# Performance work log

Measured on AMD Instinct MI355X. Metric: run time of the kernel, lower is better.

Reference implementation:

```python
import jax, jax.numpy as jnp
import numpy as np

B, L, D = 4, 2048, 64
N_HEAD = 4
LOCALITY = 0.2
PI = 3.141592653589793


def setup_inputs() -> dict:
    key = jax.random.key(0)
    k1, k2, k3 = jax.random.split(key, 3)
    mesh = jax.random.uniform(k1, (B, L, 2), dtype=jnp.float32)
    inputs = jax.random.normal(k2, (B, L, D), dtype=jnp.float32)
    lmda = jax.random.uniform(k3, (N_HEAD, 1, 1), dtype=jnp.float32)
    return {"mesh": mesh, "inputs": inputs, "lmda": lmda}


def reference(mesh, inputs, lmda):
    FMAX = jnp.finfo(jnp.float32).max
    # pairwise squared distances: (B, L, L)
    diff = mesh[:, :, None, :] - mesh[:, None, :, :]
    m_dist = jnp.sum(diff * diff, axis=-1)
    # per-head scale in (0, inf): tan(pi/4 * (1-eps) * (1 + sin(lmda)))
    scale = jnp.tan(0.25 * PI * (1.0 - 1e-07) * (1.0 + jnp.sin(lmda)))  # (H,1,1)
    scaled = m_dist[:, None, :, :] * scale  # (B, H, L, L)
    # row-wise quantile threshold (linear interpolation, matching torch.quantile)
    thresh = jnp.quantile(scaled, LOCALITY, axis=-1, keepdims=True)  # (B,H,L,1)
    masked = jnp.where(scaled <= thresh, scaled, FMAX)
    att = jax.nn.softmax(-masked, axis=-1)  # (B, H, L, L)
    # aggregate: (B,H,L,L) x (B,L,D) -> (B,L,H,D) -> (B,L,H*D)
    conv = jnp.einsum('bhnj,bjd->bnhd', att, inputs)
    conv = conv.reshape(inputs.shape[0], -1, N_HEAD * inputs.shape[-1])
    return jnp.concatenate([inputs, conv], axis=-1)
```

## Files before the change

### kernel.cpp

```cpp
#include <hip/hip_runtime.h>
#include <math.h>

#ifndef M_PI
#define M_PI 3.14159265358979323846
#endif

namespace {
constexpr int B_ = 4;
constexpr int L_ = 2048;
constexpr int D_ = 64;
constexpr int H_ = 4;
constexpr int RB = 8;
constexpr int KT = 64;
constexpr int NTILE = L_ / KT;
constexpr int CAPC = 256;
constexpr int OUTW = D_ + H_ * D_;
constexpr int APS = 2064;
}

typedef __attribute__((ext_vector_type(8))) short bf16x8;
typedef __attribute__((ext_vector_type(4))) float f32x4;

__device__ __forceinline__ unsigned bf16_rne(float x) {
    unsigned u = __float_as_uint(x);
    return (u + 0x7fffu + ((u >> 16) & 1u)) >> 16;
}

#define LDS_FENCE() __builtin_amdgcn_s_waitcnt(0xC07F)

__global__ __launch_bounds__(256) void prep_kernel(const float* __restrict__ inputs,
                                                   char* __restrict__ ws) {
    const int blk = blockIdx.x;
    const int b = blk >> 6;
    const int r6 = blk & 63;
    const int tile = r6 >> 2;
    const int qr = r6 & 3;
    const int t = threadIdx.x;
    const float* inb = inputs + ((size_t)b * L_ + tile * 128) * D_;
    char* wsb = ws + (size_t)b * (L_ * D_ * 2) + tile * (128 * D_ * 2);
    #pragma unroll
    for (int i = 0; i < 4; ++i) {
        const int idx = qr * 1024 + i * 256 + t;
        const int n  = idx & 63;
        const int kp = idx >> 6;
        const int kl = kp << 1;
        const float x0 = inb[kl * D_ + n];
        const float x1 = inb[(kl + 1) * D_ + n];
        const unsigned a = bf16_rne(x0);
        const unsigned c = bf16_rne(x1);
        const int chunk = (kl >> 3) * 64 + n;
        const int e = kl & 7;
        *reinterpret_cast<unsigned*>(wsb + chunk * 16 + e * 2) = a | (c << 16);
    }
}

__global__ __launch_bounds__(512, 8) void posatt_kernel(
    const float* __restrict__ mesh,
    const float* __restrict__ inputs,
    const float* __restrict__ lmda,
    const char* __restrict__ ws,
    float* __restrict__ out)
{
    __shared__ __align__(16) float2 s_mesh[L_];
    __shared__ __align__(16) char s_u1[16448];
    __shared__ float s_scale[H_];
    __shared__ float s_th[RB][H_];
    __shared__ float s_d409[RB], s_d410[RB];
    __shared__ float s_wsum[RB][H_];
    __shared__ unsigned s_ccw[8];

    const int t = threadIdx.x;
    const int l = t & 63;
    const int w = t >> 6;
    const int blk = blockIdx.x;
    const int b = blk >> 8;
    const int n0 = (blk & 255) * RB;

    const float2* meshg = reinterpret_cast<const float2*>(mesh) + (size_t)b * L_;

    if (t < H_) {
        const double lam = (double)lmda[t];
        const float C = (float)(0.25 * M_PI * (1.0 - 1e-07));
        const float s1 = (float)sin(lam);
        const float arg = __fmul_rn(C, __fadd_rn(1.0f, s1));
        s_scale[t] = (float)tan((double)arg);
    }
    if (t < RB) { s_d409[t] = 0.0f; s_d410[t] = 0.0f; }
    {
        const float4* mg = reinterpret_cast<const float4*>(mesh + (size_t)b * L_ * 2);
        float4* msd = reinterpret_cast<float4*>(s_mesh);
        msd[t] = mg[t];
        msd[t + 512] = mg[t + 512];
    }
    __syncthreads();

    {
        unsigned* hw = reinterpret_cast<unsigned*>(s_u1) + w * 256;
        float* cw = reinterpret_cast<float*>(s_u1 + 8192) + w * CAPC;
        const int rl = w;
        const float2 me = meshg[n0 + rl];
        *reinterpret_cast<uint4*>(&hw[l * 4]) = make_uint4(0u, 0u, 0u, 0u);
        if (l == 0) s_ccw[w] = 0u;
        LDS_FENCE();
        #pragma unroll 4
        for (int it = 0; it < 32; ++it) {
            const int j = (it << 6) + l;
            const float2 mj = meshg[j];
            const float dx = __fsub_rn(me.x, mj.x);
            const float dy = __fsub_rn(me.y, mj.y);
            const float d = __fadd_rn(__fmul_rn(dx, dx), __fmul_rn(dy, dy));
            int bin = (int)(d * 128.0f); bin = bin < 255 ? bin : 255;
            atomicAdd(&hw[bin], 1u);
        }
        LDS_FENCE();
        int lo, hi; unsigned base;
        {
            const uint4 hv = *reinterpret_cast<const uint4*>(&hw[l * 4]);
            const unsigned p0 = hv.x, p1 = p0 + hv.y, p2 = p1 + hv.z, p3 = p2 + hv.w;
            unsigned sc = p3;
            #pragma unroll
            for (int off = 1; off < 64; off <<= 1) {
                const unsigned uu = __shfl_up(sc, off);
                if (l >= off) sc += uu;
            }
            const unsigned eb = sc - p3;
            const unsigned cum[4] = {eb + p0, eb + p1, eb + p2, eb + p3};
            int flo = -1, fhi = -1; unsigned fbase = 0u;
            #pragma unroll
            for (int e = 0; e < 4; ++e) {
                const unsigned prev = e ? cum[e - 1] : eb;
                if (cum[e] > 409u && prev <= 409u) { flo = l * 4 + e; fbase = prev; }
                if (cum[e] > 410u && prev <= 410u) { fhi = l * 4 + e; }
            }
            const unsigned long long bmlo = __ballot(flo >= 0);
            const int srclo = (int)__builtin_ctzll(bmlo);
            lo = __shfl(flo, srclo);
            base = __shfl(fbase, srclo);
            const unsigned long long bmhi = __ballot(fhi >= 0);
            hi = __shfl(fhi, (int)__builtin_ctzll(bmhi));
        }
        #pragma unroll 4
        for (int it = 0; it < 32; ++it) {
            const int j = (it << 6) + l;
            const float2 mj = meshg[j];
            const float dx = __fsub_rn(me.x, mj.x);
            const float dy = __fsub_rn(me.y, mj.y);
            const float d = __fadd_rn(__fmul_rn(dx, dx), __fmul_rn(dy, dy));
            int bin = (int)(d * 128.0f); bin = bin < 255 ? bin : 255;
            if (bin >= lo && bin <= hi) {
                const unsigned p = atomicAdd(&s_ccw[w], 1u);
                if (p < (unsigned)CAPC) cw[p] = d;
            }
        }
        LDS_FENCE();
        const int m = (int)min(s_ccw[w], (unsigned)CAPC);
        const unsigned k409 = 409u - base;
        const unsigned k410 = 410u - base;
        const float lo_edge = (float)lo * 0.0078125f;
        const float sc2 = 32768.0f / (float)(hi - lo + 1);
        *reinterpret_cast<uint4*>(&hw[l * 4]) = make_uint4(0u, 0u, 0u, 0u);
        LDS_FENCE();
        #pragma unroll 2
        for (int ci = l; ci < m; ci += 64) {
            const float v = cw[ci];
            int b2 = (int)(__fmul_rn(__fsub_rn(v, lo_edge), sc2));
            b2 = b2 < 255 ? b2 : 255; b2 = b2 > 0 ? b2 : 0;
            atomicAdd(&hw[b2], 1u);
        }
        LDS_FENCE();
        int lo2, hi2; unsigned base2;
        {
            const uint4 hv = *reinterpret_cast<const uint4*>(&hw[l * 4]);
            const unsigned p0 = hv.x, p1 = p0 + hv.y, p2 = p1 + hv.z, p3 = p2 + hv.w;
            unsigned sc = p3;
            #pragma unroll
            for (int off = 1; off < 64; off <<= 1) {
                const unsigned uu = __shfl_up(sc, off);
                if (l >= off) sc += uu;
            }
            const unsigned eb = sc - p3;
            const unsigned cum[4] = {eb + p0, eb + p1, eb + p2, eb + p3};
            int flo = -1, fhi = -1; unsigned fbase = 0u;
            #pragma unroll
            for (int e = 0; e < 4; ++e) {
                const unsigned prev = e ? cum[e - 1] : eb;
                if (cum[e] > k409 && prev <= k409) { flo = l * 4 + e; fbase = prev; }
                if (cum[e] > k410 && prev <= k410) { fhi = l * 4 + e; }
            }
            const unsigned long long bmlo = __ballot(flo >= 0);
            const int srclo = (int)__builtin_ctzll(bmlo);
            lo2 = __shfl(flo, srclo);
            base2 = __shfl(fbase, srclo);
            const unsigned long long bmhi = __ballot(fhi >= 0);
            hi2 = __shfl(fhi, (int)__builtin_ctzll(bmhi));
        }
        if (l == 0) s_ccw[w] = 0u;
        LDS_FENCE();
        float* c2 = reinterpret_cast<float*>(hw);
        #pragma unroll 2
        for (int ci = l; ci < m; ci += 64) {
            const float v = cw[ci];
            int b2 = (int)(__fmul_rn(__fsub_rn(v, lo_edge), sc2));
            b2 = b2 < 255 ? b2 : 255; b2 = b2 > 0 ? b2 : 0;
            if (b2 >= lo2 && b2 <= hi2) {
                const unsigned p = atomicAdd(&s_ccw[w], 1u);
                if (p < 256u) c2[p] = v;
            }
        }
        LDS_FENCE();
        const int c = (int)min(s_ccw[w], 256u);
        const int q409 = (int)(k409 - base2);
        const int q410 = (int)(k410 - base2);
        #pragma unroll 1
        for (int cc0 = 0; cc0 < c; cc0 += 64) {
            const int ci = cc0 + l;
            const float v = (ci < c) ? c2[ci] : 0.0f;
            int lt = 0, le = 0;
            #pragma unroll 4
            for (int i = 0; i < c; ++i) {
                const float u = c2[i];
                lt += (u < v) ? 1 : 0;
                le += (u <= v) ? 1 : 0;
            }
            if (ci < c) {
                if (lt <= q409 && q409 < le) s_d409[rl] = v;
                if (lt <= q410 && q410 < le) s_d410[rl] = v;
            }
        }
    }
    __syncthreads();

    if (t < RB * H_) {
        const int r = t >> 2, h = t & 3;
        const float scl = s_scale[h];
        const float s409 = __fmul_rn(s_d409[r], scl);
        const float s410 = __fmul_rn(s_d410[r], scl);
        const float pos = 0.2f * 2047.0f;
        const float g = pos - 409.0f;
        const float lw = 1.0f - g;
        s_th[r][h] = __fadd_rn(__fmul_rn(s409, lw), __fmul_rn(s410, g));
    }
    __syncthreads();

    const int mr   = t >> 4;
    const int h_b  = mr >> 3;
    const int r_b  = mr & 7;
    const int jg   = t & 15;
    const int row16 = ((h_b & 1) << 3) + r_b;
    const int pln   = h_b >> 1;
    const float2 me_b = s_mesh[n0 + r_b];
    const float sc_b = s_scale[h_b];
    const float th_b = s_th[r_b][h_b];
    const int ks4q_w = jg >> 1;
    const int chunk_w = ks4q_w * 16 + row16;
    const int chunkSw_w = chunk_w ^ (ks4q_w & 7);
    const int aoff = pln * APS + (chunkSw_w << 4) + ((jg & 1) << 3);
    float wacc = 0.0f;

    const int p_w  = w >> 2;
    const int ks_w = (w >> 1) & 1;
    const int nqh  = w & 1;
    const int ks4q_r = ks_w * 4 + (l >> 4);
    const int chunk_r = ks4q_r * 16 + (l & 15);
    const int aroff = p_w * APS + ((chunk_r ^ (ks4q_r & 7)) << 4);
    f32x4 acc[2];
    acc[0] = (f32x4)0.0f; acc[1] = (f32x4)0.0f;

    const float* inpb = inputs + (size_t)b * L_ * D_;
    const char* wsb = ws + (size_t)b * (L_ * D_ * 2);
    char* Abase = s_u1;
    char* Bbase = s_u1 + 2 * APS;

    #pragma unroll 1
    for (int tile = 0; tile < NTILE; ++tile) {
        __syncthreads();
        const uint4 bg = *reinterpret_cast<const uint4*>(wsb + ((size_t)(tile * 512 + t) << 4));
        const int k0 = tile * KT;
        {
            const float4 mq0 = *reinterpret_cast<const float4*>(&s_mesh[k0 + jg * 4]);
            const float4 mq1 = *reinterpret_cast<const float4*>(&s_mesh[k0 + jg * 4 + 2]);
            const float dx0 = __fsub_rn(me_b.x, mq0.x);
            const float dy0 = __fsub_rn(me_b.y, mq0.y);
            const float d0 = __fadd_rn(__fmul_rn(dx0, dx0), __fmul_rn(dy0, dy0));
            const float dx1 = __fsub_rn(me_b.x, mq0.z);
            const float dy1 = __fsub_rn(me_b.y, mq0.w);
            const float d1 = __fadd_rn(__fmul_rn(dx1, dx1), __fmul_rn(dy1, dy1));
            const float dx2 = __fsub_rn(me_b.x, mq1.x);
            const float dy2 = __fsub_rn(me_b.y, mq1.y);
            const float d2 = __fadd_rn(__fmul_rn(dx2, dx2), __fmul_rn(dy2, dy2));
            const float dx3 = __fsub_rn(me_b.x, mq1.z);
            const float dy3 = __fsub_rn(me_b.y, mq1.w);
            const float d3 = __fadd_rn(__fmul_rn(dx3, dx3), __fmul_rn(dy3, dy3));
            const float x0 = __fmul_rn(d0, sc_b);
            const float x1 = __fmul_rn(d1, sc_b);
            const float x2 = __fmul_rn(d2, sc_b);
            const float x3 = __fmul_rn(d3, sc_b);
            const float w0 = (x0 <= th_b) ? __expf(-x0) : 0.0f;
            const float w1 = (x1 <= th_b) ? __expf(-x1) : 0.0f;
            const float w2 = (x2 <= th_b) ? __expf(-x2) : 0.0f;
            const float w3 = (x3 <= th_b) ? __expf(-x3) : 0.0f;
            wacc += (w0 + w1) + (w2 + w3);
            const unsigned u01 = bf16_rne(w0) | (bf16_rne(w1) << 16);
            const unsigned u23 = bf16_rne(w2) | (bf16_rne(w3) << 16);
            *reinterpret_cast<uint2*>(Abase + aoff) = make_uint2(u01, u23);
        }
        *reinterpret_cast<uint4*>(Bbase + t * 16) = bg;
        __syncthreads();
        const bf16x8 afr = *reinterpret_cast<const bf16x8*>(Abase + aroff);
        #pragma unroll
        for (int i = 0; i < 2; ++i) {
            const int nq = nqh * 2 + i;
            const bf16x8 bfr = *reinterpret_cast<const bf16x8*>(
                Bbase + (((ks_w * 4 + (l >> 4)) * 64 + nq * 16 + (l & 15)) << 4));
            acc[i] = __builtin_amdgcn_mfma_f32_16x16x32_bf16(afr, bfr, acc[i], 0, 0, 0);
        }
    }
    __syncthreads();

    wacc += __shfl_xor(wacc, 1);
    wacc += __shfl_xor(wacc, 2);
    wacc += __shfl_xor(wacc, 4);
    wacc += __shfl_xor(wacc, 8);
    if ((l & 15) == 0) s_wsum[r_b][h_b] = wacc;
    {
        float4* Cz = reinterpret_cast<float4*>(s_u1);
        Cz[t] = make_float4(0.f, 0.f, 0.f, 0.f);
    }
    __syncthreads();
    {
        float* Cf = reinterpret_cast<float*>(s_u1);
        #pragma unroll
        for (int i = 0; i < 2; ++i) {
            const int nq = nqh * 2 + i;
            #pragma unroll
            for (int reg = 0; reg < 4; ++reg) {
                const int row = (l >> 4) * 4 + reg;
                const int col = nq * 16 + (l & 15);
                atomicAdd(&Cf[(p_w * 16 + row) * 64 + col], acc[i][reg]);
            }
        }
    }
    __syncthreads();
    {
        const float* Cf = reinterpret_cast<const float*>(s_u1);
        const int pr = t >> 4;
        const int p = pr >> 4;
        const int row16o = pr & 15;
        const int h = p * 2 + (row16o >> 3);
        const int r = row16o & 7;
        const int col = (t & 15) << 2;
        const float wsv = s_wsum[r][h];
        const float inv = (wsv != 0.0f) ? 1.0f / wsv : 0.0f;
        float4 r0 = *reinterpret_cast<const float4*>(&Cf[pr * 64 + col]);
        r0.x *= inv; r0.y *= inv; r0.z *= inv; r0.w *= inv;
        float* op = out + (size_t)(b * L_ + n0 + r) * OUTW + D_ + h * 64 + col;
        *reinterpret_cast<float4*>(op) = r0;
    }
    {
        const int r = t >> 6;
        const int c = t & 63;
        out[(size_t)(b * L_ + n0 + r) * OUTW + c] = inpb[(size_t)(n0 + r) * D_ + c];
    }
}

extern "C" void kernel_launch(void* const* d_in, const int* in_sizes, int n_in,
                              void* d_out, int out_size, void* d_ws, size_t ws_size,
                              hipStream_t stream) {
    const float* mesh   = (const float*)d_in[0];
    const float* inputs = (const float*)d_in[1];
    const float* lmda   = (const float*)d_in[2];
    float* out = (float*)d_out;
    char* ws = (char*)d_ws;
    (void)in_sizes; (void)n_in; (void)out_size; (void)ws_size;
    hipLaunchKernelGGL(prep_kernel, dim3(256), dim3(256), 0, stream, inputs, ws);
    hipLaunchKernelGGL(posatt_kernel, dim3(B_ * (L_ / RB)), dim3(512), 0, stream,
                       mesh, inputs, lmda, ws, out);
}
```

Before: 132.0 us.

## Double-buffer LDS tiles and share distance math across head pairs

Uses two LDS buffers so the MFMA on one tile overlaps with building the weight tile and staging B for the next, cutting the per-tile barriers from two to one. The thread mapping is reworked so each thread computes a distance once and reuses it for two heads. The threshold is compared in unscaled distance space, and exp is replaced by exp2 with a folded log2e scale. Packed bf16 conversion uses v_cvt_pk_bf16_f32. The cost is doubled LDS use and a lower occupancy hint (6 instead of 8), and skipping the per-head scale before the threshold compare may change rounding at the boundary.

```diff
diff --git a/kernel.cpp b/kernel.cpp
--- a/kernel.cpp
+++ b/kernel.cpp
@@ -16,6 +16,9 @@
 constexpr int CAPC = 256;
 constexpr int OUTW = D_ + H_ * D_;
 constexpr int APS = 2064;
+constexpr int ABYTES = 2 * APS;
+constexpr int BBYTES = KT * D_ * 2;
+constexpr int BUFB = ABYTES + BBYTES;
 }
 
 typedef __attribute__((ext_vector_type(8))) short bf16x8;
@@ -25,6 +28,21 @@
     unsigned u = __float_as_uint(x);
     return (u + 0x7fffu + ((u >> 16) & 1u)) >> 16;
 }
+
+__device__ __forceinline__ unsigned cvt_pk_bf16(float lo, float hi) {
+    unsigned r;
+    asm("v_cvt_pk_bf16_f32 %0, %1, %2" : "=v"(r) : "v"(lo), "v"(hi));
+    return r;
+}
+
+#if defined(__has_builtin)
+#if __has_builtin(__builtin_amdgcn_exp2f)
+#define EXP2F(x) __builtin_amdgcn_exp2f(x)
+#endif
+#endif
+#ifndef EXP2F
+#define EXP2F(x) __expf((x) * 0.69314718055994531f)
+#endif
 
 #define LDS_FENCE() __builtin_amdgcn_s_waitcnt(0xC07F)
 
@@ -54,7 +72,7 @@
     }
 }
 
-__global__ __launch_bounds__(512, 8) void posatt_kernel(
+__global__ __launch_bounds__(512, 6) void posatt_kernel(
     const float* __restrict__ mesh,
     const float* __restrict__ inputs,
     const float* __restrict__ lmda,
@@ -62,9 +80,9 @@
     float* __restrict__ out)
 {
     __shared__ __align__(16) float2 s_mesh[L_];
-    __shared__ __align__(16) char s_u1[16448];
+    __shared__ __align__(16) char s_u1[2 * BUFB];
     __shared__ float s_scale[H_];
-    __shared__ float s_th[RB][H_];
+    __shared__ float s_thD[RB];
     __shared__ float s_d409[RB], s_d410[RB];
     __shared__ float s_wsum[RB][H_];
     __shared__ unsigned s_ccw[8];
@@ -230,32 +248,28 @@
     }
     __syncthreads();
 
-    if (t < RB * H_) {
-        const int r = t >> 2, h = t & 3;
-        const float scl = s_scale[h];
-        const float s409 = __fmul_rn(s_d409[r], scl);
-        const float s410 = __fmul_rn(s_d410[r], scl);
+    if (t < RB) {
         const float pos = 0.2f * 2047.0f;
         const float g = pos - 409.0f;
         const float lw = 1.0f - g;
-        s_th[r][h] = __fadd_rn(__fmul_rn(s409, lw), __fmul_rn(s410, g));
-    }
-    __syncthreads();
-
-    const int mr   = t >> 4;
-    const int h_b  = mr >> 3;
-    const int r_b  = mr & 7;
-    const int jg   = t & 15;
-    const int row16 = ((h_b & 1) << 3) + r_b;
-    const int pln   = h_b >> 1;
-    const float2 me_b = s_mesh[n0 + r_b];
-    const float sc_b = s_scale[h_b];
-    const float th_b = s_th[r_b][h_b];
-    const int ks4q_w = jg >> 1;
+        s_thD[t] = __fadd_rn(__fmul_rn(s_d409[t], lw), __fmul_rn(s_d410[t], g));
+    }
+    __syncthreads();
+
+    const int jp = t & 31;
+    const int rr = (t >> 5) & 7;
+    const int h2 = t >> 8;
+    const float2 me_b = s_mesh[n0 + rr];
+    const float thD = s_thD[rr];
+    constexpr float LOG2E = 1.4426950408889634f;
+    const float cA = __fmul_rn(-LOG2E, s_scale[h2]);
+    const float cB = __fmul_rn(-LOG2E, s_scale[h2 + 2]);
+    const int row16 = h2 * 8 + rr;
+    const int ks4q_w = jp >> 2;
     const int chunk_w = ks4q_w * 16 + row16;
     const int chunkSw_w = chunk_w ^ (ks4q_w & 7);
-    const int aoff = pln * APS + (chunkSw_w << 4) + ((jg & 1) << 3);
-    float wacc = 0.0f;
+    const int aoff0 = (chunkSw_w << 4) + ((jp & 3) << 2);
+    float waccA = 0.0f, waccB = 0.0f;
 
     const int p_w  = w >> 2;
     const int ks_w = (w >> 1) & 1;
@@ -268,60 +282,86 @@
 
     const float* inpb = inputs + (size_t)b * L_ * D_;
     const char* wsb = ws + (size_t)b * (L_ * D_ * 2);
-    char* Abase = s_u1;
-    char* Bbase = s_u1 + 2 * APS;
-
-    #pragma unroll 1
-    for (int tile = 0; tile < NTILE; ++tile) {
-        __syncthreads();
-        const uint4 bg = *reinterpret_cast<const uint4*>(wsb + ((size_t)(tile * 512 + t) << 4));
+    char* const AE = s_u1;
+    char* const BE = s_u1 + ABYTES;
+    char* const AO = s_u1 + BUFB;
+    char* const BO = s_u1 + BUFB + ABYTES;
+
+    auto LOADB = [&](int tile) -> uint4 {
+        return *reinterpret_cast<const uint4*>(wsb + ((size_t)(tile * 512 + t) << 4));
+    };
+    auto COMMITB = [&](char* Bb, const uint4 bg) {
+        *reinterpret_cast<uint4*>(Bb + (t << 4)) = bg;
+    };
+    auto ABUILD = [&](int tile, char* Ab) {
         const int k0 = tile * KT;
-        {
-            const float4 mq0 = *reinterpret_cast<const float4*>(&s_mesh[k0 + jg * 4]);
-            const float4 mq1 = *reinterpret_cast<const float4*>(&s_mesh[k0 + jg * 4 + 2]);
-            const float dx0 = __fsub_rn(me_b.x, mq0.x);
-            const float dy0 = __fsub_rn(me_b.y, mq0.y);
-            const float d0 = __fadd_rn(__fmul_rn(dx0, dx0), __fmul_rn(dy0, dy0));
-            const float dx1 = __fsub_rn(me_b.x, mq0.z);
-            const float dy1 = __fsub_rn(me_b.y, mq0.w);
-            const float d1 = __fadd_rn(__fmul_rn(dx1, dx1), __fmul_rn(dy1, dy1));
-            const float dx2 = __fsub_rn(me_b.x, mq1.x);
-            const float dy2 = __fsub_rn(me_b.y, mq1.y);
-            const float d2 = __fadd_rn(__fmul_rn(dx2, dx2), __fmul_rn(dy2, dy2));
-            const float dx3 = __fsub_rn(me_b.x, mq1.z);
-            const float dy3 = __fsub_rn(me_b.y, mq1.w);
-            const float d3 = __fadd_rn(__fmul_rn(dx3, dx3), __fmul_rn(dy3, dy3));
-            const float x0 = __fmul_rn(d0, sc_b);
-            const float x1 = __fmul_rn(d1, sc_b);
-            const float x2 = __fmul_rn(d2, sc_b);
-            const float x3 = __fmul_rn(d3, sc_b);
-            const float w0 = (x0 <= th_b) ? __expf(-x0) : 0.0f;
-            const float w1 = (x1 <= th_b) ? __expf(-x1) : 0.0f;
-            const float w2 = (x2 <= th_b) ? __expf(-x2) : 0.0f;
-            const float w3 = (x3 <= th_b) ? __expf(-x3) : 0.0f;
-            wacc += (w0 + w1) + (w2 + w3);
-            const unsigned u01 = bf16_rne(w0) | (bf16_rne(w1) << 16);
-            const unsigned u23 = bf16_rne(w2) | (bf16_rne(w3) << 16);
-            *reinterpret_cast<uint2*>(Abase + aoff) = make_uint2(u01, u23);
-        }
-        *reinterpret_cast<uint4*>(Bbase + t * 16) = bg;
-        __syncthreads();
-        const bf16x8 afr = *reinterpret_cast<const bf16x8*>(Abase + aroff);
+        const float4 mq = *reinterpret_cast<const float4*>(&s_mesh[k0 + 2 * jp]);
+        const float dx0 = __fsub_rn(me_b.x, mq.x);
+        const float dy0 = __fsub_rn(me_b.y, mq.y);
+        const float d0 = __fadd_rn(__fmul_rn(dx0, dx0), __fmul_rn(dy0, dy0));
+        const float dx1 = __fsub_rn(me_b.x, mq.z);
+        const float dy1 = __fsub_rn(me_b.y, mq.w);
+        const float d1 = __fadd_rn(__fmul_rn(dx1, dx1), __fmul_rn(dy1, dy1));
+        const bool pass0 = (d0 <= thD);
+        const bool pass1 = (d1 <= thD);
+        const float wA0 = pass0 ? EXP2F(__fmul_rn(d0, cA)) : 0.0f;
+        const float wA1 = pass1 ? EXP2F(__fmul_rn(d1, cA)) : 0.0f;
+        const float wB0 = pass0 ? EXP2F(__fmul_rn(d0, cB)) : 0.0f;
+        const float wB1 = pass1 ? EXP2F(__fmul_rn(d1, cB)) : 0.0f;
+        waccA += __fadd_rn(wA0, wA1);
+        waccB += __fadd_rn(wB0, wB1);
+        *reinterpret_cast<unsigned*>(Ab + aoff0) = cvt_pk_bf16(wA0, wA1);
+        *reinterpret_cast<unsigned*>(Ab + APS + aoff0) = cvt_pk_bf16(wB0, wB1);
+    };
+    auto MFMA_STEP = [&](const char* Ab, const char* Bb) {
+        const bf16x8 afr = *reinterpret_cast<const bf16x8*>(Ab + aroff);
         #pragma unroll
         for (int i = 0; i < 2; ++i) {
             const int nq = nqh * 2 + i;
             const bf16x8 bfr = *reinterpret_cast<const bf16x8*>(
-                Bbase + (((ks_w * 4 + (l >> 4)) * 64 + nq * 16 + (l & 15)) << 4));
+                Bb + (((ks_w * 4 + (l >> 4)) * 64 + nq * 16 + (l & 15)) << 4));
             acc[i] = __builtin_amdgcn_mfma_f32_16x16x32_bf16(afr, bfr, acc[i], 0, 0, 0);
         }
-    }
-    __syncthreads();
-
-    wacc += __shfl_xor(wacc, 1);
-    wacc += __shfl_xor(wacc, 2);
-    wacc += __shfl_xor(wacc, 4);
-    wacc += __shfl_xor(wacc, 8);
-    if ((l & 15) == 0) s_wsum[r_b][h_b] = wacc;
+    };
+
+    {
+        const uint4 bg0 = LOADB(0);
+        ABUILD(0, AE);
+        COMMITB(BE, bg0);
+    }
+    __syncthreads();
+    #pragma unroll 1
+    for (int tp = 0; tp < NTILE / 2; ++tp) {
+        uint4 bg = LOADB(2 * tp + 1);
+        MFMA_STEP(AE, BE);
+        ABUILD(2 * tp + 1, AO);
+        COMMITB(BO, bg);
+        __syncthreads();
+        if (tp < NTILE / 2 - 1) {
+            bg = LOADB(2 * tp + 2);
+            MFMA_STEP(AO, BO);
+            ABUILD(2 * tp + 2, AE);
+            COMMITB(BE, bg);
+            __syncthreads();
+        }
+    }
+    MFMA_STEP(AO, BO);
+    __syncthreads();
+
+    waccA += __shfl_xor(waccA, 1);
+    waccA += __shfl_xor(waccA, 2);
+    waccA += __shfl_xor(waccA, 4);
+    waccA += __shfl_xor(waccA, 8);
+    waccA += __shfl_xor(waccA, 16);
+    waccB += __shfl_xor(waccB, 1);
+    waccB += __shfl_xor(waccB, 2);
+    waccB += __shfl_xor(waccB, 4);
+    waccB += __shfl_xor(waccB, 8);
+    waccB += __shfl_xor(waccB, 16);
+    if ((l & 31) == 0) {
+        s_wsum[rr][h2] = waccA;
+        s_wsum[rr][h2 + 2] = waccB;
+    }
     {
         float4* Cz = reinterpret_cast<float4*>(s_u1);
         Cz[t] = make_float4(0.f, 0.f, 0.f, 0.f);
```

Result: slower. 135.5 us (+2.6%).
